# Performance work log

Measured on AMD Instinct MI355X. Metric: run time of the kernel, lower is better.

## Reference

```python
import jax, jax.numpy as jnp
import numpy as np

HEADS1, HID, LSTM_H, OUT = 4, 64, 32, 2
NEG_SLOPE = 0.2
EPS = 1e-16


def gat_layer(x, src, dst, W, att_src, att_dst, bias, heads, out_ch):
    """PyG GATConv (concat=True, add_self_loops handled by caller)."""
    N = x.shape[0]
    h = (x @ W).reshape(N, heads, out_ch)                 # [N, H, C]
    a_s = jnp.sum(h * att_src, axis=-1)                    # [N, H]
    a_d = jnp.sum(h * att_dst, axis=-1)                    # [N, H]
    e = jax.nn.leaky_relu(a_s[src] + a_d[dst], NEG_SLOPE)  # [E, H]
    m = jax.ops.segment_max(e, dst, num_segments=N)        # scatter-softmax (stable)
    e = jnp.exp(e - jax.lax.stop_gradient(m)[dst])
    denom = jax.ops.segment_sum(e, dst, num_segments=N)
    alpha = e / (denom[dst] + EPS)                         # [E, H]
    msg = h[src] * alpha[..., None]                        # [E, H, C]
    out = jax.ops.segment_sum(msg, dst, num_segments=N)    # [N, H, C]
    return out.reshape(N, heads * out_ch) + bias


def lstm_last(seq, W_ih, W_hh, b_ih, b_hh, hidden):
    """Single-layer batch_first LSTM; returns last-step hidden state. Gate order i,f,g,o (torch)."""
    B = seq.shape[0]
    xT = jnp.transpose(seq, (1, 0, 2))  # [T, B, F]
    b = b_ih + b_hh

    def step(carry, xt):
        h, c = carry
        z = xt @ W_ih.T + h @ W_hh.T + b  # [B, 4H]
        i, f, g, o = jnp.split(z, 4, axis=-1)
        c = jax.nn.sigmoid(f) * c + jax.nn.sigmoid(i) * jnp.tanh(g)
        h = jax.nn.sigmoid(o) * jnp.tanh(c)
        return (h, c), None

    h0 = jnp.zeros((B, hidden), seq.dtype)
    (h, _), _ = jax.lax.scan(step, (h0, h0), xT)
    return h


def setup_inputs() -> dict:
    key = jax.random.key(0)
    ks = jax.random.split(key, 20)
    N, E, IN, T = 50000, 800000, 128, 50
    s = lambda k, shp: jax.random.normal(k, shp, jnp.float32) * 0.05
    inp = {
        "x": jax.random.normal(ks[0], (N, IN), jnp.float32),
        "edge_index": jax.random.randint(ks[1], (2, E), 0, N, jnp.int32),
        "sequences": jax.random.normal(ks[2], (N, T, 3), jnp.float32),
        # GATConv 1: in=128 -> 64 per head, 4 heads
        "W1": s(ks[3], (IN, HEADS1 * HID)),
        "att_src1": s(ks[4], (HEADS1, HID)),
        "att_dst1": s(ks[5], (HEADS1, HID)),
        "bias1": jnp.zeros((HEADS1 * HID,), jnp.float32),
        # GATConv 2: in=256 -> 64, 1 head
        "W2": s(ks[6], (HEADS1 * HID, HID)),
        "att_src2": s(ks[7], (1, HID)),
        "att_dst2": s(ks[8], (1, HID)),
        "bias2": jnp.zeros((HID,), jnp.float32),
        # LSTM(input_size=3, hidden_size=32)
        "W_ih": s(ks[9], (4 * LSTM_H, 3)),
        "W_hh": s(ks[10], (4 * LSTM_H, LSTM_H)),
        "b_ih": jnp.zeros((4 * LSTM_H,), jnp.float32),
        "b_hh": jnp.zeros((4 * LSTM_H,), jnp.float32),
        # fusion MLP: (64+32) -> 64 -> 2
        "Wf1": s(ks[11], (HID + LSTM_H, HID)),
        "bf1": jnp.zeros((HID,), jnp.float32),
        "Wf2": s(ks[12], (HID, OUT)),
        "bf2": jnp.zeros((OUT,), jnp.float32),
    }
    return inp


def reference(x, edge_index, sequences, W1, att_src1, att_dst1, bias1,
              W2, att_src2, att_dst2, bias2, W_ih, W_hh, b_ih, b_hh,
              Wf1, bf1, Wf2, bf2):
    N = x.shape[0]
    # PyG GATConv default add_self_loops=True
    loops = jnp.arange(N, dtype=edge_index.dtype)
    src = jnp.concatenate([edge_index[0], loops])
    dst = jnp.concatenate([edge_index[1], loops])

    g = jax.nn.elu(gat_layer(x, src, dst, W1, att_src1, att_dst1, bias1, HEADS1, HID))
    # dropout is identity in eval mode
    g = gat_layer(g, src, dst, W2, att_src2, att_dst2, bias2, 1, HID)  # [N, 64]

    t = lstm_last(sequences, W_ih, W_hh, b_ih, b_hh, LSTM_H)           # [N, 32]

    combined = jnp.concatenate([g, t], axis=1)
    h = jax.nn.relu(combined @ Wf1 + bf1)
    return h @ Wf2 + bf2
```

## Files before the change

kernel.cpp:

```cpp
#include <hip/hip_runtime.h>
#include <math.h>

#define HEADS1 4
#define HID 64
#define LSTM_H 32
#define IN_F 128
#define T_STEPS 50
#define NEG_SLOPE 0.2f
#define EPS_A 1e-16f

typedef __attribute__((ext_vector_type(8))) short short8;
typedef __attribute__((ext_vector_type(4))) float floatx4;
typedef __attribute__((ext_vector_type(4))) unsigned uint32x4;

__device__ __forceinline__ float frcp(float x) {
    float r;
    asm("v_rcp_f32 %0, %1" : "=v"(r) : "v"(x));
    return r;
}
__device__ __forceinline__ float sigf(float x) { return frcp(1.0f + __expf(-x)); }
__device__ __forceinline__ float tanhfast(float x) {
    float e = __expf(2.0f * x);
    return 1.0f - 2.0f * frcp(e + 1.0f);
}
__device__ __forceinline__ unsigned short f2bf(float f) {
    unsigned u = __float_as_uint(f);
    unsigned r = (u + 0x7FFFu + ((u >> 16) & 1u)) >> 16;
    return (unsigned short)r;
}
__device__ __forceinline__ float bf2f(unsigned short s) {
    return __uint_as_float(((unsigned)s) << 16);
}
__device__ __forceinline__ unsigned cvt_pk_bf16(float a, float b) {
    unsigned r;
    asm("v_cvt_pk_bf16_f32 %0, %1, %2" : "=v"(r) : "v"(a), "v"(b));
    return r;
}
__device__ __forceinline__ float lo16f(unsigned p) { return __uint_as_float(p << 16); }
__device__ __forceinline__ float hi16f(unsigned p) { return __uint_as_float(p & 0xffff0000u); }
__device__ __forceinline__ short8 bc8(uint32x4 v) { return __builtin_bit_cast(short8, v); }

template <int KK>
__global__ void prep_wt(const float* __restrict__ W, unsigned short* __restrict__ th,
                        unsigned short* __restrict__ tl, int total, int NC) {
    int i = blockIdx.x * 256 + threadIdx.x;
    if (i >= total) return;
    int n = i / KK, k = i - n * KK;
    float v = W[k * NC + n];
    unsigned short h = f2bf(v);
    th[i] = h;
    tl[i] = f2bf(v - bf2f(h));
}

template <int K, int NC>
__global__ __launch_bounds__(256)
void gemm_mfma(const float* __restrict__ A, const unsigned short* __restrict__ Bth,
               const unsigned short* __restrict__ Btl, float* __restrict__ C, int M) {
    __shared__ float sA[128][44];
    __shared__ unsigned short sBh[64][40];
    __shared__ unsigned short sBl[64][40];
    const int tid = threadIdx.x;
    const int wave = tid >> 6, lane = tid & 63;
    const int wr = wave >> 1, wc = wave & 1;
    const int row0 = blockIdx.x * 128;
    const int col0 = blockIdx.y * 64;
    const int l15 = lane & 15, l4 = lane >> 4;

    floatx4 acc[4][2];
#pragma unroll
    for (int rb = 0; rb < 4; rb++)
#pragma unroll
        for (int cb = 0; cb < 2; cb++) acc[rb][cb] = (floatx4){0.f, 0.f, 0.f, 0.f};

    for (int k0 = 0; k0 < K; k0 += 32) {
        __syncthreads();
#pragma unroll
        for (int q = 0; q < 4; q++) {
            int idx = q * 256 + tid;
            int row = idx >> 3, seg = idx & 7;
            int gr = row0 + row;
            float4 v = (gr < M) ? *(const float4*)&A[(size_t)gr * K + k0 + seg * 4]
                                : make_float4(0.f, 0.f, 0.f, 0.f);
            *(float4*)&sA[row][seg * 4] = v;
        }
        {
            int col = tid >> 2, seg = tid & 3;
            size_t gb = (size_t)(col0 + col) * K + k0 + seg * 8;
            *(short8*)&sBh[col][seg * 8] = *(const short8*)&Bth[gb];
            *(short8*)&sBl[col][seg * 8] = *(const short8*)&Btl[gb];
        }
        __syncthreads();

        short8 bh0 = *(const short8*)&sBh[wc * 32 + 0 + l15][l4 * 8];
        short8 bl0 = *(const short8*)&sBl[wc * 32 + 0 + l15][l4 * 8];
        short8 bh1 = *(const short8*)&sBh[wc * 32 + 16 + l15][l4 * 8];
        short8 bl1 = *(const short8*)&sBl[wc * 32 + 16 + l15][l4 * 8];

#pragma unroll
        for (int rb = 0; rb < 4; rb++) {
            int row = wr * 64 + rb * 16 + l15;
            floatx4 a0 = *(const floatx4*)&sA[row][l4 * 8 + 0];
            floatx4 a1 = *(const floatx4*)&sA[row][l4 * 8 + 4];
            unsigned p0 = cvt_pk_bf16(a0[0], a0[1]);
            unsigned p1 = cvt_pk_bf16(a0[2], a0[3]);
            unsigned p2 = cvt_pk_bf16(a1[0], a1[1]);
            unsigned p3 = cvt_pk_bf16(a1[2], a1[3]);
            uint32x4 hp = {p0, p1, p2, p3};
            short8 Ah = bc8(hp);
            unsigned q0 = cvt_pk_bf16(a0[0] - lo16f(p0), a0[1] - hi16f(p0));
            unsigned q1 = cvt_pk_bf16(a0[2] - lo16f(p1), a0[3] - hi16f(p1));
            unsigned q2 = cvt_pk_bf16(a1[0] - lo16f(p2), a1[1] - hi16f(p2));
            unsigned q3 = cvt_pk_bf16(a1[2] - lo16f(p3), a1[3] - hi16f(p3));
            uint32x4 lp = {q0, q1, q2, q3};
            short8 Al = bc8(lp);

            acc[rb][0] = __builtin_amdgcn_mfma_f32_16x16x32_bf16(Ah, bh0, acc[rb][0], 0, 0, 0);
            acc[rb][0] = __builtin_amdgcn_mfma_f32_16x16x32_bf16(Ah, bl0, acc[rb][0], 0, 0, 0);
            acc[rb][0] = __builtin_amdgcn_mfma_f32_16x16x32_bf16(Al, bh0, acc[rb][0], 0, 0, 0);
            acc[rb][1] = __builtin_amdgcn_mfma_f32_16x16x32_bf16(Ah, bh1, acc[rb][1], 0, 0, 0);
            acc[rb][1] = __builtin_amdgcn_mfma_f32_16x16x32_bf16(Ah, bl1, acc[rb][1], 0, 0, 0);
            acc[rb][1] = __builtin_amdgcn_mfma_f32_16x16x32_bf16(Al, bh1, acc[rb][1], 0, 0, 0);
        }
    }

#pragma unroll
    for (int rb = 0; rb < 4; rb++)
#pragma unroll
        for (int cb = 0; cb < 2; cb++)
#pragma unroll
            for (int q = 0; q < 4; q++) {
                int row = row0 + wr * 64 + rb * 16 + l4 * 4 + q;
                int col = col0 + wc * 32 + cb * 16 + l15;
                if (row < M) C[(size_t)row * NC + col] = acc[rb][cb][q];
            }
}

__global__ void att_scores(const float* __restrict__ h, const float* __restrict__ att_s,
                           const float* __restrict__ att_d, float* __restrict__ as_,
                           float* __restrict__ ad_, int NH, int Hmask) {
    int i = blockIdx.x * blockDim.x + threadIdx.x;
    if (i >= NH) return;
    int hh = i & Hmask;
    const float* row = h + (size_t)i * HID;
    float s = 0.0f, d = 0.0f;
#pragma unroll 8
    for (int c = 0; c < HID; c++) {
        float v = row[c];
        s += v * att_s[hh * HID + c];
        d += v * att_d[hh * HID + c];
    }
    as_[i] = s;
    ad_[i] = d;
}

__global__ void count_deg(const int* __restrict__ dsts, int E, int ET, int* __restrict__ cnt) {
    int e = blockIdx.x * blockDim.x + threadIdx.x;
    if (e >= ET) return;
    int d = (e < E) ? dsts[e] : (e - E);
    atomicAdd(&cnt[d], 1);
}

__global__ void scan1(const int* __restrict__ cnt, int* __restrict__ rowp,
                      int* __restrict__ bsum, int N) {
    __shared__ int tmp[256];
    int i = blockIdx.x * 256 + threadIdx.x;
    int v = (i < N) ? cnt[i] : 0;
    tmp[threadIdx.x] = v;
    __syncthreads();
    for (int off = 1; off < 256; off <<= 1) {
        int t = (threadIdx.x >= (unsigned)off) ? tmp[threadIdx.x - off] : 0;
        __syncthreads();
        tmp[threadIdx.x] += t;
        __syncthreads();
    }
    if (i < N) rowp[i] = tmp[threadIdx.x] - v;
    if (threadIdx.x == 255) bsum[blockIdx.x] = tmp[255];
}

__global__ void scan2(int* __restrict__ bsum, int nb) {
    __shared__ int tmp[256];
    int v = (threadIdx.x < (unsigned)nb) ? bsum[threadIdx.x] : 0;
    tmp[threadIdx.x] = v;
    __syncthreads();
    for (int off = 1; off < 256; off <<= 1) {
        int t = (threadIdx.x >= (unsigned)off) ? tmp[threadIdx.x - off] : 0;
        __syncthreads();
        tmp[threadIdx.x] += t;
        __syncthreads();
    }
    if (threadIdx.x < (unsigned)nb) bsum[threadIdx.x] = tmp[threadIdx.x] - v;
}

__global__ void scan3(int* __restrict__ rowp, const int* __restrict__ bsum, int N, int ET) {
    int i = blockIdx.x * 256 + threadIdx.x;
    if (i < N) rowp[i] += bsum[blockIdx.x];
    if (i == 0) rowp[N] = ET;
}

__global__ void scatter_edges(const int* __restrict__ dsts, int E, int ET,
                              const int* __restrict__ rowp, int* __restrict__ cursor,
                              int* __restrict__ eid) {
    int e = blockIdx.x * blockDim.x + threadIdx.x;
    if (e >= ET) return;
    int d = (e < E) ? dsts[e] : (e - E);
    int pos = atomicAdd(&cursor[d], 1);
    eid[rowp[d] + pos] = e;
}

__global__ __launch_bounds__(256)
void gat_agg1_sp(const int* __restrict__ srcs, int E,
                 const int* __restrict__ rowp, const int* __restrict__ eid,
                 const float* __restrict__ as_, const float* __restrict__ ad_,
                 const float* __restrict__ hfeat, const float* __restrict__ bias,
                 float* __restrict__ g, int N) {
    __shared__ float s_alpha[4][64];
    const int wave = threadIdx.x >> 6;
    const int lane = threadIdx.x & 63;
    const int dst = blockIdx.x * 4 + wave;
    if (dst >= N) return;
    const int start = rowp[dst], end = rowp[dst + 1];
    const float adv = ad_[dst];

    float dsum = 0.0f, acc = 0.0f;
    for (int i0 = start; i0 < end; i0 += 64) {
        int cnt = min(64, end - i0);
        int i = i0 + lane;
        int s = 0;
        if (i < end) {
            int e = eid[i];
            s = (e < E) ? srcs[e] : (e - E);
            float t = as_[s] + adv;
            t = (t > 0.f) ? t : NEG_SLOPE * t;
            float ex = __expf(t);
            dsum += ex;
            s_alpha[wave][lane] = ex;
        }
        __builtin_amdgcn_wave_barrier();
#pragma unroll 4
        for (int k = 0; k < cnt; k++) {
            float a_k = s_alpha[wave][k];
            int   s_k = __shfl(s, k);
            acc += a_k * hfeat[(size_t)s_k * 64 + lane];
        }
        __builtin_amdgcn_wave_barrier();
    }
#pragma unroll
    for (int mk = 32; mk >= 1; mk >>= 1) dsum += __shfl_xor(dsum, mk);
    g[(size_t)dst * 64 + lane] = acc / (dsum + EPS_A) + bias[lane];
}

__global__ void prep_wsplit(const float* __restrict__ Wih, const float* __restrict__ Whh,
                            const float* __restrict__ bih, const float* __restrict__ bhh,
                            uint32x4* __restrict__ wsp) {
    const int tid = threadIdx.x;
    const int kk = tid >> 7, sub = (tid >> 6) & 1, lane = tid & 63;
    const int grp = lane >> 4, col = lane & 15;
    const int krow = grp * 8;
    const int n = (sub + kk * 2) * 16 + col;
    float w[8];
    *(float4*)&w[0] = *(const float4*)&Whh[n * 32 + krow + 0];
    *(float4*)&w[4] = *(const float4*)&Whh[n * 32 + krow + 4];
    unsigned hi[8], lo[8];
#pragma unroll
    for (int j = 0; j < 8; j++) {
        unsigned short hs = f2bf(w[j]);
        hi[j] = hs;
        lo[j] = f2bf(w[j] - bf2f(hs));
    }
    uint32x4 BH = {hi[0] | (hi[1] << 16), hi[2] | (hi[3] << 16),
                   hi[4] | (hi[5] << 16), hi[6] | (hi[7] << 16)};
    uint32x4 BL = {lo[0] | (lo[1] << 16), lo[2] | (lo[3] << 16),
                   lo[4] | (lo[5] << 16), lo[6] | (lo[7] << 16)};
    float wi0 = Wih[n * 3 + 0], wi1 = Wih[n * 3 + 1], wi2 = Wih[n * 3 + 2];
    float bb = bih[n] + bhh[n];
    unsigned h0 = f2bf(wi0), h1 = f2bf(wi1), h2 = f2bf(wi2), hb = f2bf(bb);
    uint32x4 B2 = {0u, 0u, 0u, 0u};
    if (grp == 0) {
        unsigned bl_ = f2bf(bb - bf2f((unsigned short)hb));
        B2[0] = h0 | (h1 << 16); B2[1] = h2 | (hb << 16);
        B2[2] = h0 | (h1 << 16); B2[3] = h2 | (bl_ << 16);
    } else if (grp == 1) {
        unsigned l0 = f2bf(wi0 - bf2f((unsigned short)h0));
        unsigned l1 = f2bf(wi1 - bf2f((unsigned short)h1));
        unsigned l2 = f2bf(wi2 - bf2f((unsigned short)h2));
        B2[0] = l0 | (l1 << 16); B2[1] = l2;
    }
    wsp[((kk * 3 + 0) * 2 + sub) * 64 + lane] = B2;
    wsp[((kk * 3 + 1) * 2 + sub) * 64 + lane] = BH;
    wsp[((kk * 3 + 2) * 2 + sub) * 64 + lane] = BL;
}

__global__ __launch_bounds__(256)
void agg4_lstm(const int* __restrict__ srcs, int E,
               const int* __restrict__ rowp, const int* __restrict__ eid,
               const float* __restrict__ as_, const float* __restrict__ ad_,
               const float* __restrict__ hfeat, const float* __restrict__ bias,
               float* __restrict__ g,
               const float* __restrict__ seq, const uint32x4* __restrict__ wsp,
               float* __restrict__ t_out, int N, int nLstm) {
    __shared__ float smem[2304];

    const int bid = blockIdx.x;
    const bool isLstm = (bid % 9 == 0) && (bid / 9 < nLstm);

    if (isLstm) {
        float (*s_h)[2][16][36] = (float(*)[2][16][36])smem;
        const int lbid = bid / 9;
        const int tid  = threadIdx.x;
        const int wave = tid >> 6, lane = tid & 63;
        const int pair = wave >> 1, sub = wave & 1;
        const int grp  = lane >> 4, col = lane & 15;
        const int node0 = lbid * 32 + pair * 16;

#define LF(KK, W) wsp[(((KK) * 3 + (W)) * 2 + sub) * 64 + lane]
        uint32x4 B2_0 = LF(0, 0), BH_0 = LF(0, 1), BL_0 = LF(0, 2);
        uint32x4 B2_1 = LF(1, 0), BH_1 = LF(1, 1), BL_1 = LF(1, 2);
        uint32x4 B2_2 = LF(2, 0), BH_2 = LF(2, 1), BL_2 = LF(2, 2);
        uint32x4 B2_3 = LF(3, 0), BH_3 = LF(3, 1), BL_3 = LF(3, 2);
#undef LF
        asm volatile("" : "+v"(B2_0), "+v"(BH_0), "+v"(BL_0),
                          "+v"(B2_1), "+v"(BH_1), "+v"(BL_1),
                          "+v"(B2_2), "+v"(BH_2), "+v"(BL_2),
                          "+v"(B2_3), "+v"(BH_3), "+v"(BL_3));

        for (int i = tid; i < 2 * 2 * 16 * 36; i += 256) smem[i] = 0.0f;
        __syncthreads();

        float cst0 = 0.f, cst1 = 0.f, cst2 = 0.f, cst3 = 0.f;
        float hn0 = 0.f, hn1 = 0.f, hn2 = 0.f, hn3 = 0.f;
        const floatx4 zac = {0.f, 0.f, 0.f, 0.f};

        const int nodeX = node0 + col;
        const bool vx = (nodeX < N) && (grp < 2);
        const bool g0 = (grp == 0);
        const float* xp = seq + (size_t)nodeX * (T_STEPS * 3);

        float xv0 = vx ? xp[0] : 0.0f;
        float xv1 = vx ? xp[1] : 0.0f;
        float xv2 = vx ? xp[2] : 0.0f;

#pragma unroll 1
        for (int t = 0; t < T_STEPS; t++) {
            unsigned w0 = cvt_pk_bf16(xv0, xv1);
            unsigned w1 = cvt_pk_bf16(xv2, g0 ? 1.0f : 0.0f);
            float e0 = xv0 - lo16f(w0);
            float e1 = xv1 - hi16f(w0);
            float e2 = xv2 - lo16f(w1);
            unsigned w2 = g0 ? cvt_pk_bf16(e0, e1) : 0u;
            unsigned w3 = g0 ? cvt_pk_bf16(e2, 1.0f) : 0u;
            uint32x4 a2p = {w0, w1, w2, w3};
            short8 A2 = bc8(a2p);

            const float* hr = &s_h[pair][(t + 1) & 1][col][grp * 8];
            floatx4 h0 = *(const floatx4*)&hr[0];
            floatx4 h1 = *(const floatx4*)&hr[4];
            unsigned p0 = cvt_pk_bf16(h0[0], h0[1]);
            unsigned p1 = cvt_pk_bf16(h0[2], h0[3]);
            unsigned p2 = cvt_pk_bf16(h1[0], h1[1]);
            unsigned p3 = cvt_pk_bf16(h1[2], h1[3]);
            uint32x4 hip = {p0, p1, p2, p3};
            short8 Ahi = bc8(hip);
            unsigned q0 = cvt_pk_bf16(h0[0] - lo16f(p0), h0[1] - hi16f(p0));
            unsigned q1 = cvt_pk_bf16(h0[2] - lo16f(p1), h0[3] - hi16f(p1));
            unsigned q2 = cvt_pk_bf16(h1[0] - lo16f(p2), h1[1] - hi16f(p2));
            unsigned q3 = cvt_pk_bf16(h1[2] - lo16f(p3), h1[3] - hi16f(p3));
            uint32x4 lop = {q0, q1, q2, q3};
            short8 Alo = bc8(lop);

            {
                int tn = (t + 1 < T_STEPS) ? (t + 1) : t;
                xv0 = vx ? xp[tn * 3 + 0] : 0.0f;
                xv1 = vx ? xp[tn * 3 + 1] : 0.0f;
                xv2 = vx ? xp[tn * 3 + 2] : 0.0f;
            }

            floatx4 d0 = __builtin_amdgcn_mfma_f32_16x16x32_bf16(A2, bc8(B2_0), zac, 0, 0, 0);
            d0 = __builtin_amdgcn_mfma_f32_16x16x32_bf16(Alo, bc8(BH_0), d0, 0, 0, 0);
            d0 = __builtin_amdgcn_mfma_f32_16x16x32_bf16(Ahi, bc8(BL_0), d0, 0, 0, 0);
            d0 = __builtin_amdgcn_mfma_f32_16x16x32_bf16(Ahi, bc8(BH_0), d0, 0, 0, 0);
            floatx4 d1 = __builtin_amdgcn_mfma_f32_16x16x32_bf16(A2, bc8(B2_1), zac, 0, 0, 0);
            d1 = __builtin_amdgcn_mfma_f32_16x16x32_bf16(Alo, bc8(BH_1), d1, 0, 0, 0);
            d1 = __builtin_amdgcn_mfma_f32_16x16x32_bf16(Ahi, bc8(BL_1), d1, 0, 0, 0);
            d1 = __builtin_amdgcn_mfma_f32_16x16x32_bf16(Ahi, bc8(BH_1), d1, 0, 0, 0);
            floatx4 d2 = __builtin_amdgcn_mfma_f32_16x16x32_bf16(A2, bc8(B2_2), zac, 0, 0, 0);
            d2 = __builtin_amdgcn_mfma_f32_16x16x32_bf16(Alo, bc8(BH_2), d2, 0, 0, 0);
            d2 = __builtin_amdgcn_mfma_f32_16x16x32_bf16(Ahi, bc8(BL_2), d2, 0, 0, 0);
            d2 = __builtin_amdgcn_mfma_f32_16x16x32_bf16(Ahi, bc8(BH_2), d2, 0, 0, 0);
            floatx4 d3 = __builtin_amdgcn_mfma_f32_16x16x32_bf16(A2, bc8(B2_3), zac, 0, 0, 0);
            d3 = __builtin_amdgcn_mfma_f32_16x16x32_bf16(Alo, bc8(BH_3), d3, 0, 0, 0);
            d3 = __builtin_amdgcn_mfma_f32_16x16x32_bf16(Ahi, bc8(BL_3), d3, 0, 0, 0);
            d3 = __builtin_amdgcn_mfma_f32_16x16x32_bf16(Ahi, bc8(BH_3), d3, 0, 0, 0);

            {
                float ig, fg, gv, og;
                ig = sigf(d0[0]); fg = sigf(d1[0]); gv = tanhfast(d2[0]); og = sigf(d3[0]);
                cst0 = fg * cst0 + ig * gv; hn0 = og * tanhfast(cst0);
                ig = sigf(d0[1]); fg = sigf(d1[1]); gv = tanhfast(d2[1]); og = sigf(d3[1]);
                cst1 = fg * cst1 + ig * gv; hn1 = og * tanhfast(cst1);
                ig = sigf(d0[2]); fg = sigf(d1[2]); gv = tanhfast(d2[2]); og = sigf(d3[2]);
                cst2 = fg * cst2 + ig * gv; hn2 = og * tanhfast(cst2);
                ig = sigf(d0[3]); fg = sigf(d1[3]); gv = tanhfast(d2[3]); og = sigf(d3[3]);
                cst3 = fg * cst3 + ig * gv; hn3 = og * tanhfast(cst3);
            }

            float* hw = &s_h[pair][t & 1][4 * grp][sub * 16 + col];
            hw[0 * 36] = hn0; hw[1 * 36] = hn1; hw[2 * 36] = hn2; hw[3 * 36] = hn3;
            __syncthreads();
        }

        {
            int node = node0 + 4 * grp;
            const int c = sub * 16 + col;
            if (node + 0 < N) t_out[(size_t)(node + 0) * LSTM_H + c] = hn0;
            if (node + 1 < N) t_out[(size_t)(node + 1) * LSTM_H + c] = hn1;
            if (node + 2 < N) t_out[(size_t)(node + 2) * LSTM_H + c] = hn2;
            if (node + 3 < N) t_out[(size_t)(node + 3) * LSTM_H + c] = hn3;
        }
        return;
    }

    {
        float (*s_alpha)[64][4] = (float(*)[64][4])smem;
        const int aid = bid - bid / 9 - 1;
        const int wave = threadIdx.x >> 6;
        const int lane = threadIdx.x & 63;
        const int head = lane >> 4;
        const int dst = aid * 4 + wave;
        if (dst >= N) return;
        const int start = rowp[dst], end = rowp[dst + 1];
        const float4 adv = ((const float4*)ad_)[dst];
        const float4* h4 = (const float4*)hfeat;

        float4 dsum = make_float4(0.f, 0.f, 0.f, 0.f);
        float4 acc  = make_float4(0.f, 0.f, 0.f, 0.f);

        for (int i0 = start; i0 < end; i0 += 64) {
            int cnt = min(64, end - i0);
            int i = i0 + lane;
            int s = 0;
            if (i < end) {
                int e = eid[i];
                s = (e < E) ? srcs[e] : (e - E);
                float4 a = ((const float4*)as_)[s];
                float tx, ex;
                tx = a.x + adv.x; tx = (tx > 0.f) ? tx : NEG_SLOPE * tx; ex = __expf(tx);
                dsum.x += ex; s_alpha[wave][lane][0] = ex;
                tx = a.y + adv.y; tx = (tx > 0.f) ? tx : NEG_SLOPE * tx; ex = __expf(tx);
                dsum.y += ex; s_alpha[wave][lane][1] = ex;
                tx = a.z + adv.z; tx = (tx > 0.f) ? tx : NEG_SLOPE * tx; ex = __expf(tx);
                dsum.z += ex; s_alpha[wave][lane][2] = ex;
                tx = a.w + adv.w; tx = (tx > 0.f) ? tx : NEG_SLOPE * tx; ex = __expf(tx);
                dsum.w += ex; s_alpha[wave][lane][3] = ex;
            }
            __builtin_amdgcn_wave_barrier();
#pragma unroll 4
            for (int k = 0; k < cnt; k++) {
                float a_k = s_alpha[wave][k][head];
                int   s_k = __shfl(s, k);
                float4 hv = h4[(size_t)s_k * 64 + lane];
                acc.x += a_k * hv.x; acc.y += a_k * hv.y;
                acc.z += a_k * hv.z; acc.w += a_k * hv.w;
            }
            __builtin_amdgcn_wave_barrier();
        }
#pragma unroll
        for (int mk = 32; mk >= 1; mk >>= 1) {
            dsum.x += __shfl_xor(dsum.x, mk);
            dsum.y += __shfl_xor(dsum.y, mk);
            dsum.z += __shfl_xor(dsum.z, mk);
            dsum.w += __shfl_xor(dsum.w, mk);
        }
        float den = (head == 0) ? dsum.x : (head == 1) ? dsum.y : (head == 2) ? dsum.z : dsum.w;
        float inv = 1.0f / (den + EPS_A);
        float4 b4 = ((const float4*)bias)[lane];
        float4 r;
        r.x = acc.x * inv + b4.x; r.x = (r.x > 0.f) ? r.x : __expf(r.x) - 1.f;
        r.y = acc.y * inv + b4.y; r.y = (r.y > 0.f) ? r.y : __expf(r.y) - 1.f;
        r.z = acc.z * inv + b4.z; r.z = (r.z > 0.f) ? r.z : __expf(r.z) - 1.f;
        r.w = acc.w * inv + b4.w; r.w = (r.w > 0.f) ? r.w : __expf(r.w) - 1.f;
        ((float4*)g)[(size_t)dst * 64 + lane] = r;
    }
}

__global__ void fusion_kernel(const float* __restrict__ g2, const float* __restrict__ tt,
                              const float* __restrict__ Wf1, const float* __restrict__ bf1,
                              const float* __restrict__ Wf2, const float* __restrict__ bf2,
                              float* __restrict__ out, int N) {
    __shared__ float sW[96 * 64];
    __shared__ float sb1[64];
    __shared__ float sW2[128];
    for (int i = threadIdx.x; i < 96 * 64; i += 256) sW[i] = Wf1[i];
    if (threadIdx.x < 64) sb1[threadIdx.x] = bf1[threadIdx.x];
    if (threadIdx.x < 128) sW2[threadIdx.x] = Wf2[threadIdx.x];
    __syncthreads();
    const int wave = threadIdx.x >> 6;
    const int lane = threadIdx.x & 63;
    for (int n = blockIdx.x * 4 + wave; n < N; n += gridDim.x * 4) {
        const float* gn = g2 + (size_t)n * 64;
        const float* tn = tt + (size_t)n * 32;
        float acc = sb1[lane];
#pragma unroll 8
        for (int k = 0; k < 64; k++) acc += gn[k] * sW[k * 64 + lane];
#pragma unroll 8
        for (int k = 0; k < 32; k++) acc += tn[k] * sW[(64 + k) * 64 + lane];
        acc = fmaxf(acc, 0.0f);
        float o0 = acc * sW2[lane * 2 + 0];
        float o1 = acc * sW2[lane * 2 + 1];
#pragma unroll
        for (int mk = 32; mk >= 1; mk >>= 1) {
            o0 += __shfl_xor(o0, mk);
            o1 += __shfl_xor(o1, mk);
        }
        if (lane == 0) {
            out[(size_t)n * 2 + 0] = o0 + bf2[0];
            out[(size_t)n * 2 + 1] = o1 + bf2[1];
        }
    }
}

extern "C" void kernel_launch(void* const* d_in, const int* in_sizes, int n_in,
                              void* d_out, int out_size, void* d_ws, size_t ws_size,
                              hipStream_t stream) {
    const float* x      = (const float*)d_in[0];
    const int*   eidx   = (const int*)d_in[1];
    const float* seq    = (const float*)d_in[2];
    const float* W1     = (const float*)d_in[3];
    const float* att_s1 = (const float*)d_in[4];
    const float* att_d1 = (const float*)d_in[5];
    const float* bias1  = (const float*)d_in[6];
    const float* W2     = (const float*)d_in[7];
    const float* att_s2 = (const float*)d_in[8];
    const float* att_d2 = (const float*)d_in[9];
    const float* bias2  = (const float*)d_in[10];
    const float* Wih    = (const float*)d_in[11];
    const float* Whh    = (const float*)d_in[12];
    const float* bih    = (const float*)d_in[13];
    const float* bhh    = (const float*)d_in[14];
    const float* Wf1    = (const float*)d_in[15];
    const float* bf1    = (const float*)d_in[16];
    const float* Wf2    = (const float*)d_in[17];
    const float* bf2    = (const float*)d_in[18];
    float* out = (float*)d_out;

    const int N  = in_sizes[0] / IN_F;
    const int E  = in_sizes[1] / 2;
    const int ET = E + N;
    const int* srcs = eidx;
    const int* dsts = eidx + E;

    float* fws = (float*)d_ws;
    size_t o = 0;
    float* h1  = fws + o; o += (size_t)N * 256;
    float* g1  = fws + o; o += (size_t)N * 256;
    float* tt  = fws + o; o += (size_t)N * 32;
    float* as1 = fws + o; o += (size_t)N * 4;
    float* ad1 = fws + o; o += (size_t)N * 4;
    int* cnt    = (int*)(fws + o);
    int* rowp   = cnt + N;
    int* cursor = rowp + N + 1;
    int* eid    = cursor + N;
    int* bsum   = eid + ET;
    uintptr_t wp_ = (uintptr_t)(bsum + 512);
    wp_ = (wp_ + 15) & ~(uintptr_t)15;
    uint32x4* wsp = (uint32x4*)wp_;
    unsigned short* w1h = (unsigned short*)(wsp + 1536);
    unsigned short* w1l = w1h + 32768;
    unsigned short* w2h = w1l + 32768;
    unsigned short* w2l = w2h + 16384;
    float* h2 = h1;
    float* g2 = h1 + (size_t)N * 64;
    float* as2 = as1; float* ad2 = ad1;

    const int nTiles = (N + 255) / 256;
    dim3 blk(256);

    hipMemsetAsync(cnt, 0, (size_t)N * sizeof(int), stream);
    hipMemsetAsync(cursor, 0, (size_t)N * sizeof(int), stream);
    count_deg<<<(ET + 255) / 256, blk, 0, stream>>>(dsts, E, ET, cnt);
    scan1<<<nTiles, blk, 0, stream>>>(cnt, rowp, bsum, N);
    scan2<<<1, blk, 0, stream>>>(bsum, nTiles);
    scan3<<<(N + 256) / 256, blk, 0, stream>>>(rowp, bsum, N, ET);
    scatter_edges<<<(ET + 255) / 256, blk, 0, stream>>>(dsts, E, ET, rowp, cursor, eid);

    prep_wsplit<<<1, 512, 0, stream>>>(Wih, Whh, bih, bhh, wsp);
    prep_wt<128><<<(32768 + 255) / 256, blk, 0, stream>>>(W1, w1h, w1l, 32768, 256);
    prep_wt<256><<<(16384 + 255) / 256, blk, 0, stream>>>(W2, w2h, w2l, 16384, 64);

    gemm_mfma<128, 256><<<dim3((N + 127) / 128, 4), blk, 0, stream>>>(x, w1h, w1l, h1, N);
    att_scores<<<(N * 4 + 255) / 256, blk, 0, stream>>>(h1, att_s1, att_d1, as1, ad1, N * 4, 3);

    {
        const int nLstm = (N + 31) / 32;
        const int nAgg  = (N + 3) / 4;
        agg4_lstm<<<nLstm + nAgg, blk, 0, stream>>>(srcs, E, rowp, eid, as1, ad1,
                                                    h1, bias1, g1, seq, wsp, tt, N, nLstm);
    }

    gemm_mfma<256, 64><<<dim3((N + 127) / 128, 1), blk, 0, stream>>>(g1, w2h, w2l, h2, N);
    att_scores<<<(N + 255) / 256, blk, 0, stream>>>(h2, att_s2, att_d2, as2, ad2, N, 0);
    gat_agg1_sp<<<(N + 3) / 4, blk, 0, stream>>>(srcs, E, rowp, eid, as2, ad2, h2, bias2, g2, N);

    fusion_kernel<<<512, blk, 0, stream>>>(g2, tt, Wf1, bf1, Wf2, bf2, out, N);
}
```

Measured before the change: 699.3 us.

## Merge degree count into GEMM1, scatter into scores, fuse layer-2 aggregation with MLP

Degree counting now runs as extra blocks of the first GEMM launch, and edge scattering runs as extra blocks of the layer-1 attention-score launch. This overlaps the CSR build with dense work and removes launches. The layer-2 aggregation is fused with the fusion MLP, so g2 is never written to or reread from global memory. The trade-off is that each aggregation block now loads the 96x64 MLP weights into shared memory, which means many redundant weight loads and higher LDS use that may lower occupancy.

```diff
diff --git a/kernel.cpp b/kernel.cpp
--- a/kernel.cpp
+++ b/kernel.cpp
@@ -135,6 +135,134 @@
             }
 }
 
+__global__ __launch_bounds__(256)
+void gemm1_count(const float* __restrict__ A, const unsigned short* __restrict__ Bth,
+                 const unsigned short* __restrict__ Btl, float* __restrict__ C, int M,
+                 const int* __restrict__ dsts, int E, int ET, int* __restrict__ cnt,
+                 int nGemmRow) {
+    __shared__ float sA[128][44];
+    __shared__ unsigned short sBh[64][40];
+    __shared__ unsigned short sBl[64][40];
+    const int bid = blockIdx.x;
+    const int nGemm = nGemmRow * 4;
+
+    if (bid >= nGemm) {
+        int e = (bid - nGemm) * 256 + threadIdx.x;
+        if (e < ET) {
+            int d = (e < E) ? dsts[e] : (e - E);
+            atomicAdd(&cnt[d], 1);
+        }
+        return;
+    }
+
+    constexpr int K = 128, NC = 256;
+    const int tid = threadIdx.x;
+    const int wave = tid >> 6, lane = tid & 63;
+    const int wr = wave >> 1, wc = wave & 1;
+    const int row0 = (bid / 4) * 128;
+    const int col0 = (bid & 3) * 64;
+    const int l15 = lane & 15, l4 = lane >> 4;
+
+    floatx4 acc[4][2];
+#pragma unroll
+    for (int rb = 0; rb < 4; rb++)
+#pragma unroll
+        for (int cb = 0; cb < 2; cb++) acc[rb][cb] = (floatx4){0.f, 0.f, 0.f, 0.f};
+
+    for (int k0 = 0; k0 < K; k0 += 32) {
+        __syncthreads();
+#pragma unroll
+        for (int q = 0; q < 4; q++) {
+            int idx = q * 256 + tid;
+            int row = idx >> 3, seg = idx & 7;
+            int gr = row0 + row;
+            float4 v = (gr < M) ? *(const float4*)&A[(size_t)gr * K + k0 + seg * 4]
+                                : make_float4(0.f, 0.f, 0.f, 0.f);
+            *(float4*)&sA[row][seg * 4] = v;
+        }
+        {
+            int col = tid >> 2, seg = tid & 3;
+            size_t gb = (size_t)(col0 + col) * K + k0 + seg * 8;
+            *(short8*)&sBh[col][seg * 8] = *(const short8*)&Bth[gb];
+            *(short8*)&sBl[col][seg * 8] = *(const short8*)&Btl[gb];
+        }
+        __syncthreads();
+
+        short8 bh0 = *(const short8*)&sBh[wc * 32 + 0 + l15][l4 * 8];
+        short8 bl0 = *(const short8*)&sBl[wc * 32 + 0 + l15][l4 * 8];
+        short8 bh1 = *(const short8*)&sBh[wc * 32 + 16 + l15][l4 * 8];
+        short8 bl1 = *(const short8*)&sBl[wc * 32 + 16 + l15][l4 * 8];
+
+#pragma unroll
+        for (int rb = 0; rb < 4; rb++) {
+            int row = wr * 64 + rb * 16 + l15;
+            floatx4 a0 = *(const floatx4*)&sA[row][l4 * 8 + 0];
+            floatx4 a1 = *(const floatx4*)&sA[row][l4 * 8 + 4];
+            unsigned p0 = cvt_pk_bf16(a0[0], a0[1]);
+            unsigned p1 = cvt_pk_bf16(a0[2], a0[3]);
+            unsigned p2 = cvt_pk_bf16(a1[0], a1[1]);
+            unsigned p3 = cvt_pk_bf16(a1[2], a1[3]);
+            uint32x4 hp = {p0, p1, p2, p3};
+            short8 Ah = bc8(hp);
+            unsigned q0 = cvt_pk_bf16(a0[0] - lo16f(p0), a0[1] - hi16f(p0));
+            unsigned q1 = cvt_pk_bf16(a0[2] - lo16f(p1), a0[3] - hi16f(p1));
+            unsigned q2 = cvt_pk_bf16(a1[0] - lo16f(p2), a1[1] - hi16f(p2));
+            unsigned q3 = cvt_pk_bf16(a1[2] - lo16f(p3), a1[3] - hi16f(p3));
+            uint32x4 lp = {q0, q1, q2, q3};
+            short8 Al = bc8(lp);
+
+            acc[rb][0] = __builtin_amdgcn_mfma_f32_16x16x32_bf16(Ah, bh0, acc[rb][0], 0, 0, 0);
+            acc[rb][0] = __builtin_amdgcn_mfma_f32_16x16x32_bf16(Ah, bl0, acc[rb][0], 0, 0, 0);
+            acc[rb][0] = __builtin_amdgcn_mfma_f32_16x16x32_bf16(Al, bh0, acc[rb][0], 0, 0, 0);
+            acc[rb][1] = __builtin_amdgcn_mfma_f32_16x16x32_bf16(Ah, bh1, acc[rb][1], 0, 0, 0);
+            acc[rb][1] = __builtin_amdgcn_mfma_f32_16x16x32_bf16(Ah, bl1, acc[rb][1], 0, 0, 0);
+            acc[rb][1] = __builtin_amdgcn_mfma_f32_16x16x32_bf16(Al, bh1, acc[rb][1], 0, 0, 0);
+        }
+    }
+
+#pragma unroll
+    for (int rb = 0; rb < 4; rb++)
+#pragma unroll
+        for (int cb = 0; cb < 2; cb++)
+#pragma unroll
+            for (int q = 0; q < 4; q++) {
+                int row = row0 + wr * 64 + rb * 16 + l4 * 4 + q;
+                int col = col0 + wc * 32 + cb * 16 + l15;
+                if (row < M) C[(size_t)row * 256 + col] = acc[rb][cb][q];
+            }
+}
+
+__global__ void sc1_scatter(const float* __restrict__ h, const float* __restrict__ att_s,
+                            const float* __restrict__ att_d, float* __restrict__ as_,
+                            float* __restrict__ ad_, int NH,
+                            const int* __restrict__ dsts, int E, int ET,
+                            const int* __restrict__ rowp, int* __restrict__ cursor,
+                            int* __restrict__ eid, int nScore) {
+    const int bid = blockIdx.x;
+    if (bid >= nScore) {
+        int e = (bid - nScore) * 256 + threadIdx.x;
+        if (e < ET) {
+            int d = (e < E) ? dsts[e] : (e - E);
+            int pos = atomicAdd(&cursor[d], 1);
+            eid[rowp[d] + pos] = e;
+        }
+        return;
+    }
+    int i = bid * 256 + threadIdx.x;
+    if (i >= NH) return;
+    int hh = i & 3;
+    const float* row = h + (size_t)i * HID;
+    float s = 0.0f, d = 0.0f;
+#pragma unroll 8
+    for (int c = 0; c < HID; c++) {
+        float v = row[c];
+        s += v * att_s[hh * HID + c];
+        d += v * att_d[hh * HID + c];
+    }
+    as_[i] = s;
+    ad_[i] = d;
+}
+
 __global__ void att_scores(const float* __restrict__ h, const float* __restrict__ att_s,
                            const float* __restrict__ att_d, float* __restrict__ as_,
                            float* __restrict__ ad_, int NH, int Hmask) {
@@ -153,13 +281,6 @@
     ad_[i] = d;
 }
 
-__global__ void count_deg(const int* __restrict__ dsts, int E, int ET, int* __restrict__ cnt) {
-    int e = blockIdx.x * blockDim.x + threadIdx.x;
-    if (e >= ET) return;
-    int d = (e < E) ? dsts[e] : (e - E);
-    atomicAdd(&cnt[d], 1);
-}
-
 __global__ void scan1(const int* __restrict__ cnt, int* __restrict__ rowp,
                       int* __restrict__ bsum, int N) {
     __shared__ int tmp[256];
@@ -195,58 +316,6 @@
     int i = blockIdx.x * 256 + threadIdx.x;
     if (i < N) rowp[i] += bsum[blockIdx.x];
     if (i == 0) rowp[N] = ET;
-}
-
-__global__ void scatter_edges(const int* __restrict__ dsts, int E, int ET,
-                              const int* __restrict__ rowp, int* __restrict__ cursor,
-                              int* __restrict__ eid) {
-    int e = blockIdx.x * blockDim.x + threadIdx.x;
-    if (e >= ET) return;
-    int d = (e < E) ? dsts[e] : (e - E);
-    int pos = atomicAdd(&cursor[d], 1);
-    eid[rowp[d] + pos] = e;
-}
-
-__global__ __launch_bounds__(256)
-void gat_agg1_sp(const int* __restrict__ srcs, int E,
-                 const int* __restrict__ rowp, const int* __restrict__ eid,
-                 const float* __restrict__ as_, const float* __restrict__ ad_,
-                 const float* __restrict__ hfeat, const float* __restrict__ bias,
-                 float* __restrict__ g, int N) {
-    __shared__ float s_alpha[4][64];
-    const int wave = threadIdx.x >> 6;
-    const int lane = threadIdx.x & 63;
-    const int dst = blockIdx.x * 4 + wave;
-    if (dst >= N) return;
-    const int start = rowp[dst], end = rowp[dst + 1];
-    const float adv = ad_[dst];
-
-    float dsum = 0.0f, acc = 0.0f;
-    for (int i0 = start; i0 < end; i0 += 64) {
-        int cnt = min(64, end - i0);
-        int i = i0 + lane;
-        int s = 0;
-        if (i < end) {
-            int e = eid[i];
-            s = (e < E) ? srcs[e] : (e - E);
-            float t = as_[s] + adv;
-            t = (t > 0.f) ? t : NEG_SLOPE * t;
-            float ex = __expf(t);
-            dsum += ex;
-            s_alpha[wave][lane] = ex;
-        }
-        __builtin_amdgcn_wave_barrier();
-#pragma unroll 4
-        for (int k = 0; k < cnt; k++) {
-            float a_k = s_alpha[wave][k];
-            int   s_k = __shfl(s, k);
-            acc += a_k * hfeat[(size_t)s_k * 64 + lane];
-        }
-        __builtin_amdgcn_wave_barrier();
-    }
-#pragma unroll
-    for (int mk = 32; mk >= 1; mk >>= 1) dsum += __shfl_xor(dsum, mk);
-    g[(size_t)dst * 64 + lane] = acc / (dsum + EPS_A) + bias[lane];
 }
 
 __global__ void prep_wsplit(const float* __restrict__ Wih, const float* __restrict__ Whh,
@@ -482,10 +551,16 @@
     }
 }
 
-__global__ void fusion_kernel(const float* __restrict__ g2, const float* __restrict__ tt,
-                              const float* __restrict__ Wf1, const float* __restrict__ bf1,
-                              const float* __restrict__ Wf2, const float* __restrict__ bf2,
-                              float* __restrict__ out, int N) {
+__global__ __launch_bounds__(256)
+void agg1_mlp(const int* __restrict__ srcs, int E,
+              const int* __restrict__ rowp, const int* __restrict__ eid,
+              const float* __restrict__ as_, const float* __restrict__ ad_,
+              const float* __restrict__ hfeat, const float* __restrict__ bias,
+              const float* __restrict__ tt,
+              const float* __restrict__ Wf1, const float* __restrict__ bf1,
+              const float* __restrict__ Wf2, const float* __restrict__ bf2,
+              float* __restrict__ out, int N) {
+    __shared__ float s_alpha[4][64];
     __shared__ float sW[96 * 64];
     __shared__ float sb1[64];
     __shared__ float sW2[128];
@@ -493,28 +568,58 @@
     if (threadIdx.x < 64) sb1[threadIdx.x] = bf1[threadIdx.x];
     if (threadIdx.x < 128) sW2[threadIdx.x] = Wf2[threadIdx.x];
     __syncthreads();
+
     const int wave = threadIdx.x >> 6;
     const int lane = threadIdx.x & 63;
-    for (int n = blockIdx.x * 4 + wave; n < N; n += gridDim.x * 4) {
-        const float* gn = g2 + (size_t)n * 64;
-        const float* tn = tt + (size_t)n * 32;
-        float acc = sb1[lane];
+    const int dst = blockIdx.x * 4 + wave;
+    if (dst >= N) return;
+    const int start = rowp[dst], end = rowp[dst + 1];
+    const float adv = ad_[dst];
+
+    float dsum = 0.0f, acc = 0.0f;
+    for (int i0 = start; i0 < end; i0 += 64) {
+        int cnt = min(64, end - i0);
+        int i = i0 + lane;
+        int s = 0;
+        if (i < end) {
+            int e = eid[i];
+            s = (e < E) ? srcs[e] : (e - E);
+            float t = as_[s] + adv;
+            t = (t > 0.f) ? t : NEG_SLOPE * t;
+            float ex = __expf(t);
+            dsum += ex;
+            s_alpha[wave][lane] = ex;
+        }
+        __builtin_amdgcn_wave_barrier();
+#pragma unroll 4
+        for (int k = 0; k < cnt; k++) {
+            float a_k = s_alpha[wave][k];
+            int   s_k = __shfl(s, k);
+            acc += a_k * hfeat[(size_t)s_k * 64 + lane];
+        }
+        __builtin_amdgcn_wave_barrier();
+    }
+#pragma unroll
+    for (int mk = 32; mk >= 1; mk >>= 1) dsum += __shfl_xor(dsum, mk);
+    const float gval = acc / (dsum + EPS_A) + bias[lane];
+
+    float tval = (lane < 32) ? tt[(size_t)dst * 32 + lane] : 0.0f;
+    float m = sb1[lane];
 #pragma unroll 8
-        for (int k = 0; k < 64; k++) acc += gn[k] * sW[k * 64 + lane];
+    for (int k = 0; k < 64; k++) m += __shfl(gval, k) * sW[k * 64 + lane];
 #pragma unroll 8
-        for (int k = 0; k < 32; k++) acc += tn[k] * sW[(64 + k) * 64 + lane];
-        acc = fmaxf(acc, 0.0f);
-        float o0 = acc * sW2[lane * 2 + 0];
-        float o1 = acc * sW2[lane * 2 + 1];
-#pragma unroll
-        for (int mk = 32; mk >= 1; mk >>= 1) {
-            o0 += __shfl_xor(o0, mk);
-            o1 += __shfl_xor(o1, mk);
-        }
-        if (lane == 0) {
-            out[(size_t)n * 2 + 0] = o0 + bf2[0];
-            out[(size_t)n * 2 + 1] = o1 + bf2[1];
-        }
+    for (int k = 0; k < 32; k++) m += __shfl(tval, k) * sW[(64 + k) * 64 + lane];
+    m = fmaxf(m, 0.0f);
+    float o0 = m * sW2[lane * 2 + 0];
+    float o1 = m * sW2[lane * 2 + 1];
+#pragma unroll
+    for (int mk = 32; mk >= 1; mk >>= 1) {
+        o0 += __shfl_xor(o0, mk);
+        o1 += __shfl_xor(o1, mk);
+    }
+    if (lane == 0) {
+        out[(size_t)dst * 2 + 0] = o0 + bf2[0];
+        out[(size_t)dst * 2 + 1] = o1 + bf2[1];
     }
 }
 
@@ -568,7 +673,6 @@
     unsigned short* w2h = w1l + 32768;
     unsigned short* w2l = w2h + 16384;
     float* h2 = h1;
-    float* g2 = h1 + (size_t)N * 64;
     float* as2 = as1; float* ad2 = ad1;
 
     const int nTiles = (N + 255) / 256;
@@ -576,18 +680,28 @@
 
     hipMemsetAsync(cnt, 0, (size_t)N * sizeof(int), stream);
     hipMemsetAsync(cursor, 0, (size_t)N * sizeof(int), stream);
-    count_deg<<<(ET + 255) / 256, blk, 0, stream>>>(dsts, E, ET, cnt);
+
+    prep_wsplit<<<1, 512, 0, stream>>>(Wih, Whh, bih, bhh, wsp);
+    prep_wt<128><<<(32768 + 255) / 256, blk, 0, stream>>>(W1, w1h, w1l, 32768, 256);
+    prep_wt<256><<<(16384 + 255) / 256, blk, 0, stream>>>(W2, w2h, w2l, 16384, 64);
+
+    {
+        const int nGemmRow = (N + 127) / 128;
+        const int nCount   = (ET + 255) / 256;
+        gemm1_count<<<nGemmRow * 4 + nCount, blk, 0, stream>>>(
+            x, w1h, w1l, h1, N, dsts, E, ET, cnt, nGemmRow);
+    }
+
     scan1<<<nTiles, blk, 0, stream>>>(cnt, rowp, bsum, N);
     scan2<<<1, blk, 0, stream>>>(bsum, nTiles);
     scan3<<<(N + 256) / 256, blk, 0, stream>>>(rowp, bsum, N, ET);
-    scatter_edges<<<(ET + 255) / 256, blk, 0, stream>>>(dsts, E, ET, rowp, cursor, eid);
-
-    prep_wsplit<<<1, 512, 0, stream>>>(Wih, Whh, bih, bhh, wsp);
-    prep_wt<128><<<(32768 + 255) / 256, blk, 0, stream>>>(W1, w1h, w1l, 32768, 256);
-    prep_wt<256><<<(16384 + 255) / 256, blk, 0, stream>>>(W2, w2h, w2l, 16384, 64);
-
-    gemm_mfma<128, 256><<<dim3((N + 127) / 128, 4), blk, 0, stream>>>(x, w1h, w1l, h1, N);
-    att_scores<<<(N * 4 + 255) / 256, blk, 0, stream>>>(h1, att_s1, att_d1, as1, ad1, N * 4, 3);
+
+    {
+        const int nScore = (N * 4 + 255) / 256;
+        const int nScat  = (ET + 255) / 256;
+        sc1_scatter<<<nScore + nScat, blk, 0, stream>>>(
+            h1, att_s1, att_d1, as1, ad1, N * 4, dsts, E, ET, rowp, cursor, eid, nScore);
+    }
 
     {
         const int nLstm = (N + 31) / 32;
@@ -598,7 +712,7 @@
 
     gemm_mfma<256, 64><<<dim3((N + 127) / 128, 1), blk, 0, stream>>>(g1, w2h, w2l, h2, N);
     att_scores<<<(N + 255) / 256, blk, 0, stream>>>(h2, att_s2, att_d2, as2, ad2, N, 0);
-    gat_agg1_sp<<<(N + 3) / 4, blk, 0, stream>>>(srcs, E, rowp, eid, as2, ad2, h2, bias2, g2, N);
-
-    fusion_kernel<<<512, blk, 0, stream>>>(g2, tt, Wf1, bf1, Wf2, bf2, out, N);
-}
+
+    agg1_mlp<<<(N + 3) / 4, blk, 0, stream>>>(srcs, E, rowp, eid, as2, ad2, h2, bias2,
+                                              tt, Wf1, bf1, Wf2, bf2, out, N);
+}
```

After: 696.5 us. Within noise of the previous version (-0.4%).
